# Optimization experiments

Measured on AMD Instinct MI355X. Metric: run time of the kernel, lower is better.

## Reference

```python
import jax, jax.numpy as jnp
import numpy as np

B, N, IN_DIM, H, D = 2, 512, 64, 8, 8  # batch, nodes, in_dim, num_heads, out_dim
NEG_BIG = 1e24  # matches torch's 1e+24 masking constant


def setup_inputs() -> dict:
    key = jax.random.key(0)
    k = jax.random.split(key, 7)
    h = jax.random.normal(k[0], (B, N, IN_DIM), dtype=jnp.float32)
    e_att = jax.random.normal(k[1], (B, N, N, H * D), dtype=jnp.float32)
    e_value = jax.random.normal(k[2], (B, N, N, H * D), dtype=jnp.float32)
    attn_mask = jax.random.uniform(k[3], (B, N, N)) > 0.2  # bool adjacency mask
    scale = 0.1
    WQ = jax.random.normal(k[4], (H * D, IN_DIM), dtype=jnp.float32) * scale
    WK = jax.random.normal(k[5], (H * D, IN_DIM), dtype=jnp.float32) * scale
    WV = jax.random.normal(k[6], (H * D, IN_DIM), dtype=jnp.float32) * scale
    return {"h": h, "e_att": e_att, "e_value": e_value, "attn_mask": attn_mask,
            "WQ": WQ, "WK": WK, "WV": WV}


def reference(h, e_att, e_value, attn_mask, WQ, WK, WV):
    b, n, _ = h.shape
    # Q, K, V projections (no bias); K pre-scaled by out_dim**-0.5
    Q = (h @ WQ.T).reshape(b, n, H, D)
    K = (h @ WK.T).reshape(b, n, H, D) * (float(D) ** -0.5)
    V = (h @ WV.T).reshape(b, n, H, D)
    # QK^T scores: [B,H,N,N] -> broadcast channel dim -> [B,H,1,N,N]
    scores = jnp.einsum('bihd,bjhd->bhij', Q, K)[:, :, None]
    mask_f = attn_mask.astype(jnp.float32)
    scores = scores - NEG_BIG * (1.0 - mask_f)[:, None, None]  # mask non-edges
    # per-channel edge bias: [B,N,N,H*D] -> [B,H,D,N,N]
    Ea = e_att.reshape(b, n, n, H, D).transpose(0, 3, 4, 1, 2)
    scores = jax.nn.softmax(scores + Ea, axis=-1)  # [B,H,D,N,N]
    # attn_dropout p=0.0 -> dropout(mask) == mask
    scores = scores * mask_f[:, None, None]
    # weighted node-value sum: sum_j scores[b,h,d,i,j] * V[b,j,h,d]
    out = jnp.einsum('bhdij,bjhd->bhdi', scores, V)
    # edge-value aggregation
    Ev = e_value.reshape(b, n, n, H, D).transpose(0, 3, 4, 1, 2)
    out = out + jnp.sum(scores * Ev, axis=-1)  # [B,H,D,N]
    # reshape to [B, N, H*D] (matches torch reshape(B, H*D, N).transpose(1,2))
    return out.reshape(b, H * D, n).transpose(0, 2, 1)
```

## Files before the change

kernel.cpp:

```cpp
#include <hip/hip_runtime.h>
#include <math.h>

#define BB 2
#define NN 512
#define IND 64
#define HH 8
#define DD 8
#define CC 64
#define QUADS 16
#define JSLOTS 32
#define JITERS (NN / JSLOTS)
#define NWAVES 8

typedef float f4 __attribute__((ext_vector_type(4)));

__global__ __launch_bounds__(64)
void qkv_kernel(const float* __restrict__ h,
                const float* __restrict__ WQ,
                const float* __restrict__ WK,
                const float* __restrict__ WV,
                float* __restrict__ Qw,
                float* __restrict__ Kw,
                float* __restrict__ Vw) {
    int bi = blockIdx.x;
    int c  = threadIdx.x;
    __shared__ float hrow[IND];
    hrow[c] = h[bi * IND + c];
    __syncthreads();
    float aq = 0.f, ak = 0.f, av = 0.f;
#pragma unroll
    for (int k = 0; k < IND; ++k) {
        float hv = hrow[k];
        aq += hv * WQ[c * IND + k];
        ak += hv * WK[c * IND + k];
        av += hv * WV[c * IND + k];
    }
    Qw[bi * CC + c] = aq;
    Kw[bi * CC + c] = ak * 0.35355339059327376f;
    Vw[bi * CC + c] = av;
}

__global__ __launch_bounds__(512, 4)
void attn_kernel(const float* __restrict__ e_att,
                 const float* __restrict__ e_value,
                 const int*   __restrict__ mask,
                 const float* __restrict__ Qw,
                 const float* __restrict__ Kw,
                 const float* __restrict__ Vw,
                 float* __restrict__ out) {
    int bi  = blockIdx.x;
    int b   = bi >> 9;
    int tid = threadIdx.x;
    int q   = tid & 15;
    int jg  = tid >> 4;
    int wv  = tid >> 6;
    int hh  = q >> 1;

    __shared__ float  Qrow[CC];
    __shared__ float  qk_s[NN * HH];
    __shared__ float  maskf[NN];
    __shared__ float4 wred_l[NWAVES][QUADS];
    __shared__ float4 wred_a[NWAVES][QUADS];

    if (tid < CC) Qrow[tid] = Qw[bi * CC + tid];
    {
        const int* mrow = mask + (size_t)bi * NN;
        maskf[tid] = mrow[tid] ? 1.f : 0.f;
    }
    __syncthreads();

    const float* Kb = Kw + (size_t)b * NN * CC;
    const float* Vb = Vw + (size_t)b * NN * CC;

#pragma unroll
    for (int e = tid; e < NN * HH; e += 512) {
        int j = e >> 3, h = e & 7;
        const float* kr = Kb + (size_t)j * CC + h * 8;
        float k0[4], k1[4];
        *(float4*)k0 = *(const float4*)(kr);
        *(float4*)k1 = *(const float4*)(kr + 4);
        float s = 0.f;
#pragma unroll
        for (int d = 0; d < 4; ++d) s += Qrow[h * 8 + d] * k0[d];
#pragma unroll
        for (int d = 0; d < 4; ++d) s += Qrow[h * 8 + 4 + d] * k1[d];
        qk_s[e] = s;
    }
    __syncthreads();

    const f4* ea_row = (const f4*)(e_att   + (size_t)bi * NN * CC) + q;
    const f4* ev_row = (const f4*)(e_value + (size_t)bi * NN * CC) + q;
    const f4* v_col  = (const f4*)Vb + q;

    float l[4] = {0.f, 0.f, 0.f, 0.f};
    float a[4] = {0.f, 0.f, 0.f, 0.f};

#pragma unroll 4
    for (int it = 0; it < JITERS; ++it) {
        int j = it * JSLOTS + jg;
        f4 ea4 = __builtin_nontemporal_load(ea_row + (size_t)j * QUADS);
        f4 ev4 = __builtin_nontemporal_load(ev_row + (size_t)j * QUADS);
        f4 vv4 = v_col[(size_t)j * QUADS];
        float qk  = qk_s[j * HH + hh];
        float msk = maskf[j];
#pragma unroll
        for (int cc = 0; cc < 4; ++cc) {
            float s = fminf(qk + ea4[cc], 30.f);
            float p = msk * __expf(s);
            l[cc] += p;
            a[cc] += p * (vv4[cc] + ev4[cc]);
        }
    }

#pragma unroll
    for (int off = 16; off <= 32; off <<= 1) {
#pragma unroll
        for (int cc = 0; cc < 4; ++cc) {
            l[cc] += __shfl_xor(l[cc], off, 64);
            a[cc] += __shfl_xor(a[cc], off, 64);
        }
    }
    if ((tid & 63) < QUADS) {
        wred_l[wv][q] = make_float4(l[0], l[1], l[2], l[3]);
        wred_a[wv][q] = make_float4(a[0], a[1], a[2], a[3]);
    }
    __syncthreads();

    if (tid < CC) {
        int cq = tid >> 2, sub = tid & 3;
        float L = 0.f, A = 0.f;
#pragma unroll
        for (int w = 0; w < NWAVES; ++w) {
            L += ((const float*)&wred_l[w][cq])[sub];
            A += ((const float*)&wred_a[w][cq])[sub];
        }
        out[(size_t)bi * CC + tid] = (L > 0.f) ? (A / L) : 0.f;
    }
}

extern "C" void kernel_launch(void* const* d_in, const int* in_sizes, int n_in,
                              void* d_out, int out_size, void* d_ws, size_t ws_size,
                              hipStream_t stream) {
    const float* h       = (const float*)d_in[0];
    const float* e_att   = (const float*)d_in[1];
    const float* e_value = (const float*)d_in[2];
    const int*   mask    = (const int*)  d_in[3];
    const float* WQ      = (const float*)d_in[4];
    const float* WK      = (const float*)d_in[5];
    const float* WV      = (const float*)d_in[6];
    float* out = (float*)d_out;

    float* Qw = (float*)d_ws;
    float* Kw = Qw + (size_t)BB * NN * CC;
    float* Vw = Kw + (size_t)BB * NN * CC;

    qkv_kernel<<<BB * NN, 64, 0, stream>>>(h, WQ, WK, WV, Qw, Kw, Vw);
    attn_kernel<<<BB * NN, 512, 0, stream>>>(e_att, e_value, mask, Qw, Kw, Vw, out);
}
```

Measured before the change: 61.43 us.

## Compact masked-in neighbor indices and skip loads for masked-out edges

```diff
diff --git a/kernel.cpp b/kernel.cpp
--- a/kernel.cpp
+++ b/kernel.cpp
@@ -9,7 +9,6 @@
 #define CC 64
 #define QUADS 16
 #define JSLOTS 32
-#define JITERS (NN / JSLOTS)
 #define NWAVES 8
 
 typedef float f4 __attribute__((ext_vector_type(4)));
@@ -58,16 +57,29 @@
 
     __shared__ float  Qrow[CC];
     __shared__ float  qk_s[NN * HH];
-    __shared__ float  maskf[NN];
+    __shared__ int    jlist[NN];
+    __shared__ int    wtot[NWAVES], woff[NWAVES];
+    __shared__ int    nvalid_s;
     __shared__ float4 wred_l[NWAVES][QUADS];
     __shared__ float4 wred_a[NWAVES][QUADS];
 
     if (tid < CC) Qrow[tid] = Qw[bi * CC + tid];
-    {
-        const int* mrow = mask + (size_t)bi * NN;
-        maskf[tid] = mrow[tid] ? 1.f : 0.f;
+    jlist[tid] = 0;
+
+    int valid = mask[(size_t)bi * NN + tid] != 0;
+    unsigned long long ball = __ballot(valid);
+    int lane = tid & 63;
+    int rank = __popcll(ball & ((1ull << lane) - 1ull));
+    if (lane == 0) wtot[wv] = __popcll(ball);
+    __syncthreads();
+    if (tid == 0) {
+        int s = 0;
+#pragma unroll
+        for (int w = 0; w < NWAVES; ++w) { woff[w] = s; s += wtot[w]; }
+        nvalid_s = s;
     }
     __syncthreads();
+    if (valid) jlist[woff[wv] + rank] = tid;
 
     const float* Kb = Kw + (size_t)b * NN * CC;
     const float* Vb = Vw + (size_t)b * NN * CC;
@@ -92,23 +104,29 @@
     const f4* ev_row = (const f4*)(e_value + (size_t)bi * NN * CC) + q;
     const f4* v_col  = (const f4*)Vb + q;
 
+    int nvalid = nvalid_s;
+    int nblk   = (nvalid + 127) >> 7;
+
     float l[4] = {0.f, 0.f, 0.f, 0.f};
     float a[4] = {0.f, 0.f, 0.f, 0.f};
 
-#pragma unroll 4
-    for (int it = 0; it < JITERS; ++it) {
-        int j = it * JSLOTS + jg;
-        f4 ea4 = __builtin_nontemporal_load(ea_row + (size_t)j * QUADS);
-        f4 ev4 = __builtin_nontemporal_load(ev_row + (size_t)j * QUADS);
-        f4 vv4 = v_col[(size_t)j * QUADS];
-        float qk  = qk_s[j * HH + hh];
-        float msk = maskf[j];
+    for (int blk = 0; blk < nblk; ++blk) {
 #pragma unroll
-        for (int cc = 0; cc < 4; ++cc) {
-            float s = fminf(qk + ea4[cc], 30.f);
-            float p = msk * __expf(s);
-            l[cc] += p;
-            a[cc] += p * (vv4[cc] + ev4[cc]);
+        for (int u = 0; u < 4; ++u) {
+            int idx = blk * 128 + u * JSLOTS + jg;
+            int j   = jlist[idx];
+            float w = (idx < nvalid) ? 1.f : 0.f;
+            f4 ea4 = ea_row[(size_t)j * QUADS];
+            f4 ev4 = ev_row[(size_t)j * QUADS];
+            f4 vv4 = v_col [(size_t)j * QUADS];
+            float qk = qk_s[j * HH + hh];
+#pragma unroll
+            for (int cc = 0; cc < 4; ++cc) {
+                float s = fminf(qk + ea4[cc], 30.f);
+                float p = w * __expf(s);
+                l[cc] += p;
+                a[cc] += p * (vv4[cc] + ev4[cc]);
+            }
         }
     }
 
```

After: 49.45 us, median of 2. 1.24x faster.
